# Kernel optimization log

Measured on AMD Instinct MI355X. Metric: run time of the kernel, lower is better.

## Reference

```python
import jax, jax.numpy as jnp
import numpy as np
import math

B, LAT, HID, T, NCLS = 128, 128, 256, 1920, 3
EPS = 1e-5


def _ln(x, g, b):
    m = jnp.mean(x, axis=-1, keepdims=True)
    v = jnp.var(x, axis=-1, keepdims=True)
    return (x - m) * jax.lax.rsqrt(v + EPS) * g + b


def _leaky(x):
    return jax.nn.leaky_relu(x, 0.2)


def _lstm_layer(x, Wih, Whh, bih, bhh):
    # x: [T, B, D] time-major; gate order i,f,g,o (PyTorch convention)
    xw = jnp.einsum('tbd,gd->tbg', x, Wih) + bih + bhh  # precompute input projection
    Hd = Whh.shape[1]
    bsz = x.shape[1]

    def step(carry, xg):
        h, c = carry
        gates = xg + h @ Whh.T
        i, f, g, o = jnp.split(gates, 4, axis=-1)
        c = jax.nn.sigmoid(f) * c + jax.nn.sigmoid(i) * jnp.tanh(g)
        h = jax.nn.sigmoid(o) * jnp.tanh(c)
        return (h, c), h

    init = (jnp.zeros((bsz, Hd), x.dtype), jnp.zeros((bsz, Hd), x.dtype))
    _, hs = jax.lax.scan(step, init, xw)
    return hs  # [T, B, H]


def setup_inputs() -> dict:
    key = jax.random.key(0)
    ks = jax.random.split(key, 16)
    s = 0.05
    H2 = HID // 2
    d = {
        'z': jax.random.normal(ks[0], (B, LAT), jnp.float32),
        'labels': jax.random.randint(ks[1], (B,), 0, 4, jnp.int64),
        'emb_W': jax.random.normal(ks[2], (NCLS + 1, HID), jnp.float32) * s,
        'np_W': jax.random.normal(ks[3], (HID, LAT + HID), jnp.float32) * s,
        'np_b': jnp.zeros((HID,), jnp.float32),
        'np_g': jnp.ones((HID,), jnp.float32),
        'np_be': jnp.zeros((HID,), jnp.float32),
        'Wih0': jax.random.normal(ks[4], (4 * HID, 2 * HID), jnp.float32) * s,
        'Whh0': jax.random.normal(ks[5], (4 * HID, HID), jnp.float32) * s,
        'bih0': jnp.zeros((4 * HID,), jnp.float32),
        'bhh0': jnp.zeros((4 * HID,), jnp.float32),
        'Wih1': jax.random.normal(ks[6], (4 * HID, HID), jnp.float32) * s,
        'Whh1': jax.random.normal(ks[7], (4 * HID, HID), jnp.float32) * s,
        'bih1': jnp.zeros((4 * HID,), jnp.float32),
        'bhh1': jnp.zeros((4 * HID,), jnp.float32),
        'oW1': jax.random.normal(ks[8], (H2, HID), jnp.float32) * s,
        'ob1': jnp.zeros((H2,), jnp.float32),
        'og': jnp.ones((H2,), jnp.float32),
        'obe': jnp.zeros((H2,), jnp.float32),
        'oW2': jax.random.normal(ks[9], (3, H2), jnp.float32) * s,
        'ob2': jnp.zeros((3,), jnp.float32),
        'sW1': jax.random.normal(ks[10], (H2, HID), jnp.float32) * s,
        'sb1': jnp.zeros((H2,), jnp.float32),
        'sg': jnp.ones((H2,), jnp.float32),
        'sbe': jnp.zeros((H2,), jnp.float32),
        'sW2': jax.random.normal(ks[11], (1, H2), jnp.float32) * s,
        'sb2': jnp.zeros((1,), jnp.float32),
        'stress_w': jnp.array(1.8, jnp.float32),
        'amu_w': jnp.array([0.15, 0.7, 0.15], jnp.float32),
        'amu_b': jnp.array(-0.3, jnp.float32),
    }
    return d


def reference(z, labels, emb_W, np_W, np_b, np_g, np_be, Wih0, Whh0, bih0, bhh0,
              Wih1, Whh1, bih1, bhh1, oW1, ob1, og, obe, oW2, ob2,
              sW1, sb1, sg, sbe, sW2, sb2, stress_w, amu_w, amu_b):
    bsz = z.shape[0]
    emb = emb_W[labels]                                   # [B, H]
    h = _leaky(_ln(jnp.concatenate([z, emb], axis=1) @ np_W.T + np_b, np_g, np_be))
    # [B, T, 2H]
    sig_in = jnp.concatenate([
        jnp.broadcast_to(h[:, None, :], (bsz, T, HID)),
        jnp.broadcast_to(emb[:, None, :], (bsz, T, HID)),
    ], axis=2)
    x = jnp.transpose(sig_in, (1, 0, 2))                  # time-major [T, B, 2H]
    x = _lstm_layer(x, Wih0, Whh0, bih0, bhh0)
    x = _lstm_layer(x, Wih1, Whh1, bih1, bhh1)
    ch = jnp.transpose(x, (1, 0, 2))                      # [B, T, H]

    # oscillation params per sample (vectorized over batch)
    h_avg = jnp.mean(ch, axis=1)                          # [B, H]
    op = _leaky(_ln(h_avg @ oW1.T + ob1, og, obe)) @ oW2.T + ob2  # [B, 3]
    freq = 0.23 + 0.04 * jnp.tanh(op[:, 0])
    amp = 2.0 + 1.5 * jnp.tanh(op[:, 1])
    phase = math.pi * jax.nn.sigmoid(op[:, 2])
    t = jnp.linspace(0.0, 1.0, T)
    osc = amp[:, None] * jnp.sin(2.0 * math.pi * freq[:, None] * T * t[None, :] + phase[:, None])  # [B, T]

    base = jnp.tanh(_leaky(_ln(ch @ sW1.T + sb1, sg, sbe)) @ sW2.T + sb2)  # [B, T, 1]
    enhanced = 0.6 * base[..., 0] + 0.4 * osc             # [B, T]

    stressed = stress_w * enhanced                        # conv1d k=1, w=1.8
    xp = jnp.pad(enhanced, ((0, 0), (1, 1)))
    smoothed = amu_w[0] * xp[:, :-2] + amu_w[1] * xp[:, 1:-1] + amu_w[2] * xp[:, 2:] + amu_b

    lab = labels[:, None]
    out = jnp.where(lab == 1, enhanced,
          jnp.where(lab == 2, stressed,
          jnp.where(lab == 3, smoothed, jnp.zeros_like(enhanced))))
    return out[..., None]                                  # [B, T, 1]
```

## Files before the change

kernel.cpp:

```cpp
#include <hip/hip_runtime.h>

#define TSTEPS 1920
#define NB 128
#define HIDN 256
#define LATN 128
#define EPSF 1e-5f

typedef __attribute__((ext_vector_type(8))) short bf16x8;
typedef __attribute__((ext_vector_type(4))) float f32x4;

__device__ __forceinline__ unsigned short f2bf(float x) {
    unsigned u = __builtin_bit_cast(unsigned, x);
    unsigned r = (u + 0x7fffu + ((u >> 16) & 1u)) >> 16;
    return (unsigned short)r;
}
__device__ __forceinline__ float bf2f(unsigned short h) {
    unsigned u = ((unsigned)h) << 16;
    return __builtin_bit_cast(float, u);
}
__device__ __forceinline__ float fsig(float x) {
    float e = __expf(-fabsf(x));
    float s = 1.f / (1.f + e);
    return x >= 0.f ? s : 1.f - s;
}
__device__ __forceinline__ float ftanh(float x) {
    float e = __expf(-2.f * fabsf(x));
    float r = (1.f - e) / (1.f + e);
    return x >= 0.f ? r : -r;
}
__device__ __forceinline__ float fleaky(float x) { return x > 0.f ? x : 0.2f * x; }
__device__ __forceinline__ bf16x8 bcast16(uint4 v) { return __builtin_bit_cast(bf16x8, v); }

__device__ __forceinline__ unsigned aload(const unsigned* p) {
    return __hip_atomic_load(p, __ATOMIC_RELAXED, __HIP_MEMORY_SCOPE_AGENT);
}
__device__ __forceinline__ void astore(unsigned* p, unsigned v) {
    __hip_atomic_store(p, v, __ATOMIC_RELAXED, __HIP_MEMORY_SCOPE_AGENT);
}

#define MFMA(a, b, c) __builtin_amdgcn_mfma_f32_16x16x32_bf16((a), (b), (c), 0, 0, 0)

#define FLG(ph, g, s) (((ph) * 8 + (g)) * 8 + (s)) * 32
#define HPLANE(g, layer, buf) (((g) * 2 + (layer)) * 2 + (buf)) * 4096

__global__ void init_sync(unsigned* hbuf, unsigned* flags) {
    int i = blockIdx.x * 256 + threadIdx.x;
    if (i < 131072) hbuf[i] = 0u;
    if (i < 4096) flags[i] = 0u;
}

__global__ void pack_bfrag_sliced(const float* __restrict__ A, const float* __restrict__ Bsrc,
                                  int KA, int KB,
                                  unsigned short* __restrict__ hi, unsigned short* __restrict__ lo) {
    int e = blockIdx.x * 256 + threadIdx.x;
    int K = KA + KB;
    int KT = K >> 5;
    if (e >= 1024 * K) return;
    int j = e & 7;
    int l = (e >> 3) & 63;
    int r = e >> 9;
    int kt = r % KT;
    int r2 = r / KT;
    int v = r2 & 7;
    int w = r2 >> 3;
    int n = (v >> 1) * 256 + 32 * w + 16 * (v & 1) + (l & 15);
    int k = kt * 32 + (l >> 4) * 8 + j;
    float val = (k < KA) ? A[n * KA + k] : Bsrc[n * KB + (k - KA)];
    unsigned short h = f2bf(val);
    hi[e] = h;
    lo[e] = f2bf(val - bf2f(h));
}

__global__ void pack_sw1kj(const float* __restrict__ sW1, unsigned short* __restrict__ out) {
    int e = blockIdx.x * 256 + threadIdx.x;
    if (e >= 256 * 128) return;
    int j = e & 127, k = e >> 7;
    out[e] = f2bf(sW1[j * 256 + k]);
}

__global__ void pack4T(const float* __restrict__ W, int N, int K, float* __restrict__ out) {
    int e = blockIdx.x * 256 + threadIdx.x;
    if (e >= N * K) return;
    int j = e & 3;
    int rest = e >> 2;
    int n = rest % N;
    int k4 = rest / N;
    out[e] = W[n * K + 4 * k4 + j];
}

__global__ void prep_b1(const float* __restrict__ bih1, const float* __restrict__ bhh1,
                        float* __restrict__ b1sum) {
    int i = blockIdx.x * 256 + threadIdx.x;
    if (i < 1024) b1sum[i] = bih1[i] + bhh1[i];
}

__global__ void np_head(const float* __restrict__ z, const int* __restrict__ labels,
                        const float* __restrict__ emb_W, const float* __restrict__ np_W,
                        const float* __restrict__ np_b, const float* __restrict__ np_g,
                        const float* __restrict__ np_be, float* __restrict__ x_const) {
    int b = blockIdx.x;
    int j = threadIdx.x;
    __shared__ float xc[LATN + HIDN];
    __shared__ float red[8];
    int lab = labels[b];
    if (j < LATN) xc[j] = z[b * LATN + j];
    float e = emb_W[lab * HIDN + j];
    xc[LATN + j] = e;
    __syncthreads();
    float d = np_b[j];
    for (int k = 0; k < LATN + HIDN; ++k) d += xc[k] * np_W[j * (LATN + HIDN) + k];
    int lane = j & 63, wv = j >> 6;
    float s = d, s2 = d * d;
    for (int o = 1; o < 64; o <<= 1) { s += __shfl_xor(s, o); s2 += __shfl_xor(s2, o); }
    if (lane == 0) { red[wv] = s; red[4 + wv] = s2; }
    __syncthreads();
    float S = red[0] + red[1] + red[2] + red[3];
    float S2 = red[4] + red[5] + red[6] + red[7];
    float m = S * (1.f / 256.f);
    float var = S2 * (1.f / 256.f) - m * m;
    float h = fleaky((d - m) * rsqrtf(var + EPSF) * np_g[j] + np_be[j]);
    x_const[b * 512 + j] = h;
    x_const[b * 512 + 256 + j] = e;
}

__global__ void __launch_bounds__(1024) xw0_kernel(const float* __restrict__ x_const,
                                                   const float4* __restrict__ Wih0T4,
                                                   const float* __restrict__ bih0,
                                                   const float* __restrict__ bhh0,
                                                   float* __restrict__ xw0) {
    int b = blockIdx.x;
    int g = threadIdx.x;
    __shared__ float xc[512];
    if (g < 512) xc[g] = x_const[b * 512 + g];
    __syncthreads();
    const float4* xc4 = (const float4*)xc;
    float4 acc = {0.f, 0.f, 0.f, 0.f};
#pragma unroll 8
    for (int k4 = 0; k4 < 128; ++k4) {
        float4 w = Wih0T4[k4 * 1024 + g];
        float4 x = xc4[k4];
        acc.x = fmaf(w.x, x.x, acc.x);
        acc.y = fmaf(w.y, x.y, acc.y);
        acc.z = fmaf(w.z, x.z, acc.z);
        acc.w = fmaf(w.w, x.w, acc.w);
    }
    xw0[b * 1024 + g] = bih0[g] + bhh0[g] + ((acc.x + acc.y) + (acc.z + acc.w));
}

__global__ void __launch_bounds__(512, 2) lstm_coop(
    const uint4* __restrict__ whh0h, const uint4* __restrict__ whh0l,
    const uint4* __restrict__ w1h, const uint4* __restrict__ w1l,
    const unsigned short* __restrict__ sw1kj_g, const float* __restrict__ xw0g,
    const float* __restrict__ b1sum, const float* __restrict__ sb1,
    const float* __restrict__ sg, const float* __restrict__ sbe,
    const float* __restrict__ sW2, const float* __restrict__ sb2,
    unsigned* __restrict__ hbuf, unsigned* __restrict__ flags,
    float* __restrict__ base_out, float* __restrict__ hsum_out) {
    extern __shared__ char smem[];
    unsigned short* hhi = (unsigned short*)smem;
    unsigned short* hlo = (unsigned short*)(smem + 16384);
    unsigned short* sw1s = (unsigned short*)(smem + 32768);
    float* gatesL = (float*)(smem + 98304);
    float* ppart = (float*)(smem + 106752);
    char* hhiB = smem;
    char* hloB = smem + 16384;

    const int gidx = blockIdx.x & 7;
    const int W = blockIdx.x >> 3;
    const int g16 = gidx * 16;
    const int tid = threadIdx.x;
    const int l = tid & 63;
    const int v = tid >> 6;
    const int ln16 = l & 15;
    const int kg = l >> 4;

    for (int i = tid; i < 256 * 128; i += 512) sw1s[i] = sw1kj_g[i];
    for (int i = tid; i < 8192; i += 512) { hhi[i] = 0; hlo[i] = 0; }

    uint4 b0h[8], b0l[8];
#pragma unroll
    for (int kt = 0; kt < 8; ++kt) {
        int idx = ((W * 8 + v) * 8 + kt) * 64 + l;
        b0h[kt] = whh0h[idx];
        b0l[kt] = whh0l[idx];
    }
    const uint4* w1hb = w1h + ((W * 8 + v) * 16) * 64 + l;
    const uint4* w1lb = w1l + ((W * 8 + v) * 16) * 64 + l;

    const int row = tid >> 5;
    const int ul = tid & 31;
    const int ug = 32 * W + ul;
    float xwi[4], b1v[4];
#pragma unroll
    for (int gt = 0; gt < 4; ++gt) {
        xwi[gt] = xw0g[(g16 + row) * 1024 + gt * 256 + ug];
        b1v[gt] = b1sum[gt * 256 + ug];
    }
    float c0 = 0.f, c1 = 0.f, hs = 0.f;

    const float sb1a = sb1[l], sb1b = sb1[64 + l];
    const float sga = sg[l], sgb = sg[64 + l];
    const float sbea = sbe[l], sbeb = sbe[64 + l];
    const float sw2a = sW2[l], sw2b = sW2[64 + l];
    const float sb2v = sb2[0];

    unsigned* h0buf[2] = {hbuf + HPLANE(gidx, 0, 0), hbuf + HPLANE(gidx, 0, 1)};
    unsigned* h1buf[2] = {hbuf + HPLANE(gidx, 1, 0), hbuf + HPLANE(gidx, 1, 1)};
    unsigned* fl0 = flags + FLG(0, gidx, W);
    unsigned* fl1 = flags + FLG(1, gidx, W);
    unsigned* fl0base = flags + FLG(0, gidx, 0);
    unsigned* fl1base = flags + FLG(1, gidx, 0);

    const int abase = ln16 * 1024;
    const int aswz = (ln16 & 7) << 4;
    const int kgo = kg * 16;
    const int gcol = (v >> 1) * 32 + (v & 1) * 16 + ln16;
    const int hprow = 2 * W + (v & 1);
    const int hpswz = (hprow & 7) << 4;
    const int kq = v >> 1;

    __syncthreads();

    for (int t = 0; t < TSTEPS; ++t) {
        const int cur = t & 1, prev = cur ^ 1;
        {
            unsigned* src = h1buf[prev];
            for (int i = tid; i < 4096; i += 512) {
                int r_ = i >> 8, u_ = i & 255;
                unsigned val = aload(src + i);
                int off = r_ * 1024 + ((512 + 2 * u_) ^ ((r_ & 7) << 4));
                *(unsigned short*)(hhiB + off) = (unsigned short)(val >> 16);
                *(unsigned short*)(hloB + off) = (unsigned short)(val & 0xffffu);
            }
        }
        __syncthreads();
        {
            f32x4 acc = {0.f, 0.f, 0.f, 0.f};
#pragma unroll
            for (int kt = 0; kt < 8; ++kt) {
                int aoff = abase + ((kt * 64 + kgo) ^ aswz);
                bf16x8 ahi = bcast16(*(const uint4*)(hhiB + aoff));
                bf16x8 alo = bcast16(*(const uint4*)(hloB + aoff));
                bf16x8 bh = bcast16(b0h[kt]);
                bf16x8 bl = bcast16(b0l[kt]);
                acc = MFMA(ahi, bh, acc);
                acc = MFMA(alo, bh, acc);
                acc = MFMA(ahi, bl, acc);
            }
#pragma unroll
            for (int r = 0; r < 4; ++r) gatesL[(kg * 4 + r) * 132 + gcol] = acc[r];
        }
        if (t > 0) {
            float accA = 0.f, accB = 0.f;
            int hb = hprow * 1024;
#pragma unroll 4
            for (int k = kq * 64; k < kq * 64 + 64; ++k) {
                int off = hb + ((512 + 2 * k) ^ hpswz);
                float h = bf2f(*(const unsigned short*)(hhiB + off)) +
                          bf2f(*(const unsigned short*)(hloB + off));
                float wA = bf2f(sw1s[k * 128 + l]);
                float wB = bf2f(sw1s[k * 128 + 64 + l]);
                accA = fmaf(wA, h, accA);
                accB = fmaf(wB, h, accB);
            }
            ppart[(v & 1) * 512 + kq * 128 + l] = accA;
            ppart[(v & 1) * 512 + kq * 128 + 64 + l] = accB;
        }
        __syncthreads();
        {
            float i_ = gatesL[row * 132 + ul] + xwi[0];
            float f_ = gatesL[row * 132 + 32 + ul] + xwi[1];
            float g_ = gatesL[row * 132 + 64 + ul] + xwi[2];
            float o_ = gatesL[row * 132 + 96 + ul] + xwi[3];
            c0 = fsig(f_) * c0 + fsig(i_) * ftanh(g_);
            float h = fsig(o_) * ftanh(c0);
            unsigned short hh = f2bf(h);
            unsigned short ll = f2bf(h - bf2f(hh));
            astore(h0buf[cur] + row * 256 + ug, ((unsigned)hh << 16) | (unsigned)ll);
        }
        asm volatile("s_waitcnt vmcnt(0)" ::: "memory");
        __syncthreads();
        if (tid == 0) astore(fl0, (unsigned)(t + 1));
        {
            unsigned tgt = (unsigned)(t + 1);
            while (true) {
                unsigned val = (l < 8) ? aload(fl0base + l * 32) : tgt;
                if (__all((int)(val >= tgt))) break;
                __builtin_amdgcn_s_sleep(1);
            }
        }
        asm volatile("" ::: "memory");
        {
            unsigned* src = h0buf[cur];
            for (int i = tid; i < 4096; i += 512) {
                int r_ = i >> 8, u_ = i & 255;
                unsigned val = aload(src + i);
                int off = r_ * 1024 + ((2 * u_) ^ ((r_ & 7) << 4));
                *(unsigned short*)(hhiB + off) = (unsigned short)(val >> 16);
                *(unsigned short*)(hloB + off) = (unsigned short)(val & 0xffffu);
            }
        }
        __syncthreads();
        {
            f32x4 acc = {0.f, 0.f, 0.f, 0.f};
#pragma unroll 4
            for (int kt = 0; kt < 16; ++kt) {
                int aoff = abase + ((kt * 64 + kgo) ^ aswz);
                bf16x8 ahi = bcast16(*(const uint4*)(hhiB + aoff));
                bf16x8 alo = bcast16(*(const uint4*)(hloB + aoff));
                bf16x8 bh = bcast16(w1hb[kt * 64]);
                bf16x8 bl = bcast16(w1lb[kt * 64]);
                acc = MFMA(ahi, bh, acc);
                acc = MFMA(alo, bh, acc);
                acc = MFMA(ahi, bl, acc);
            }
#pragma unroll
            for (int r = 0; r < 4; ++r) gatesL[(kg * 4 + r) * 132 + gcol] = acc[r];
        }
        __syncthreads();
        {
            float i_ = gatesL[row * 132 + ul] + b1v[0];
            float f_ = gatesL[row * 132 + 32 + ul] + b1v[1];
            float g_ = gatesL[row * 132 + 64 + ul] + b1v[2];
            float o_ = gatesL[row * 132 + 96 + ul] + b1v[3];
            c1 = fsig(f_) * c1 + fsig(i_) * ftanh(g_);
            float h = fsig(o_) * ftanh(c1);
            hs += h;
            unsigned short hh = f2bf(h);
            unsigned short ll = f2bf(h - bf2f(hh));
            astore(h1buf[cur] + row * 256 + ug, ((unsigned)hh << 16) | (unsigned)ll);
        }
        if (t > 0 && v < 2) {
            float sA = sb1a, sB = sb1b;
#pragma unroll
            for (int q = 0; q < 4; ++q) {
                sA += ppart[v * 512 + q * 128 + l];
                sB += ppart[v * 512 + q * 128 + 64 + l];
            }
            float ssum = sA + sB, ssq = sA * sA + sB * sB;
#pragma unroll
            for (int o = 1; o < 64; o <<= 1) { ssum += __shfl_xor(ssum, o); ssq += __shfl_xor(ssq, o); }
            float m = ssum * (1.f / 128.f);
            float var = ssq * (1.f / 128.f) - m * m;
            float rstd = rsqrtf(var + EPSF);
            float p0 = fleaky((sA - m) * rstd * sga + sbea);
            float p1 = fleaky((sB - m) * rstd * sgb + sbeb);
            float q = p0 * sw2a + p1 * sw2b;
#pragma unroll
            for (int o = 1; o < 64; o <<= 1) q += __shfl_xor(q, o);
            if (l == 0) base_out[(g16 + 2 * W + v) * TSTEPS + (t - 1)] = ftanh(q + sb2v);
        }
        asm volatile("s_waitcnt vmcnt(0)" ::: "memory");
        __syncthreads();
        if (tid == 0) astore(fl1, (unsigned)(t + 1));
        {
            unsigned tgt = (unsigned)(t + 1);
            while (true) {
                unsigned val = (l < 8) ? aload(fl1base + l * 32) : tgt;
                if (__all((int)(val >= tgt))) break;
                __builtin_amdgcn_s_sleep(1);
            }
        }
        asm volatile("" ::: "memory");
    }
    {
        unsigned* src = h1buf[(TSTEPS - 1) & 1];
        for (int i = tid; i < 4096; i += 512) {
            int r_ = i >> 8, u_ = i & 255;
            unsigned val = aload(src + i);
            int off = r_ * 1024 + ((512 + 2 * u_) ^ ((r_ & 7) << 4));
            *(unsigned short*)(hhiB + off) = (unsigned short)(val >> 16);
            *(unsigned short*)(hloB + off) = (unsigned short)(val & 0xffffu);
        }
    }
    __syncthreads();
    {
        float accA = 0.f, accB = 0.f;
        int hb = hprow * 1024;
#pragma unroll 4
        for (int k = kq * 64; k < kq * 64 + 64; ++k) {
            int off = hb + ((512 + 2 * k) ^ hpswz);
            float h = bf2f(*(const unsigned short*)(hhiB + off)) +
                      bf2f(*(const unsigned short*)(hloB + off));
            accA = fmaf(bf2f(sw1s[k * 128 + l]), h, accA);
            accB = fmaf(bf2f(sw1s[k * 128 + 64 + l]), h, accB);
        }
        ppart[(v & 1) * 512 + kq * 128 + l] = accA;
        ppart[(v & 1) * 512 + kq * 128 + 64 + l] = accB;
    }
    __syncthreads();
    if (v < 2) {
        float sA = sb1a, sB = sb1b;
#pragma unroll
        for (int q = 0; q < 4; ++q) {
            sA += ppart[v * 512 + q * 128 + l];
            sB += ppart[v * 512 + q * 128 + 64 + l];
        }
        float ssum = sA + sB, ssq = sA * sA + sB * sB;
#pragma unroll
        for (int o = 1; o < 64; o <<= 1) { ssum += __shfl_xor(ssum, o); ssq += __shfl_xor(ssq, o); }
        float m = ssum * (1.f / 128.f);
        float var = ssq * (1.f / 128.f) - m * m;
        float rstd = rsqrtf(var + EPSF);
        float p0 = fleaky((sA - m) * rstd * sga + sbea);
        float p1 = fleaky((sB - m) * rstd * sgb + sbeb);
        float q = p0 * sw2a + p1 * sw2b;
#pragma unroll
        for (int o = 1; o < 64; o <<= 1) q += __shfl_xor(q, o);
        if (l == 0) base_out[(g16 + 2 * W + v) * TSTEPS + (TSTEPS - 1)] = ftanh(q + sb2v);
    }
    hsum_out[(g16 + row) * HIDN + ug] = hs;
}

__global__ void out_kernel(const float* __restrict__ hsum, const float* __restrict__ oW1,
                           const float* __restrict__ ob1, const float* __restrict__ og,
                           const float* __restrict__ obe, const float* __restrict__ oW2,
                           const float* __restrict__ ob2, const float* __restrict__ base,
                           const int* __restrict__ labels, const float* __restrict__ stress_w,
                           const float* __restrict__ amu_w, const float* __restrict__ amu_b,
                           float* __restrict__ out) {
    int b = blockIdx.x;
    int tid = threadIdx.x;
    int lane = tid & 63, wv = tid >> 6;
    __shared__ float havg[256];
    __shared__ float red[8];
    __shared__ float params[3];
    __shared__ float e_row[TSTEPS];
    havg[tid] = hsum[b * 256 + tid] * (1.f / (float)TSTEPS);
    __syncthreads();
    float d1 = 0.f;
    if (tid < 128) {
        d1 = ob1[tid];
        for (int k = 0; k < 256; ++k) d1 += havg[k] * oW1[tid * 256 + k];
    }
    float s = d1, s2 = d1 * d1;
    for (int o = 1; o < 64; o <<= 1) { s += __shfl_xor(s, o); s2 += __shfl_xor(s2, o); }
    if (lane == 0 && wv < 2) { red[wv] = s; red[2 + wv] = s2; }
    __syncthreads();
    float m = (red[0] + red[1]) * (1.f / 128.f);
    float var = (red[2] + red[3]) * (1.f / 128.f) - m * m;
    float rstd = rsqrtf(var + EPSF);
    float p = 0.f;
    if (tid < 128) p = fleaky((d1 - m) * rstd * og[tid] + obe[tid]);
    float q0 = tid < 128 ? p * oW2[0 * 128 + tid] : 0.f;
    float q1 = tid < 128 ? p * oW2[1 * 128 + tid] : 0.f;
    float q2 = tid < 128 ? p * oW2[2 * 128 + tid] : 0.f;
    for (int o = 1; o < 64; o <<= 1) {
        q0 += __shfl_xor(q0, o); q1 += __shfl_xor(q1, o); q2 += __shfl_xor(q2, o);
    }
    __syncthreads();
    if (lane == 0 && wv < 2) { red[wv] = q0; red[2 + wv] = q1; red[4 + wv] = q2; }
    __syncthreads();
    if (tid == 0) {
        float op0 = red[0] + red[1] + ob2[0];
        float op1 = red[2] + red[3] + ob2[1];
        float op2 = red[4] + red[5] + ob2[2];
        params[0] = 0.23f + 0.04f * ftanh(op0);
        params[1] = 2.0f + 1.5f * ftanh(op1);
        params[2] = 3.14159265358979f * fsig(op2);
    }
    __syncthreads();
    float freq = params[0], amp = params[1], ph = params[2];
    for (int t = tid; t < TSTEPS; t += 256) {
        float x = freq * ((float)TSTEPS * (float)t / (float)(TSTEPS - 1));
        x -= floorf(x);
        float osc = amp * __sinf(6.28318530717958647f * x + ph);
        e_row[t] = 0.6f * base[b * TSTEPS + t] + 0.4f * osc;
    }
    __syncthreads();
    int lab = labels[b];
    float sw = stress_w[0];
    float w0 = amu_w[0], w1 = amu_w[1], w2 = amu_w[2], ab = amu_b[0];
    for (int t = tid; t < TSTEPS; t += 256) {
        float e = e_row[t];
        float r;
        if (lab == 1) r = e;
        else if (lab == 2) r = sw * e;
        else if (lab == 3) {
            float em = t > 0 ? e_row[t - 1] : 0.f;
            float ep = t < TSTEPS - 1 ? e_row[t + 1] : 0.f;
            r = w0 * em + w1 * e + w2 * ep + ab;
        } else r = 0.f;
        out[b * TSTEPS + t] = r;
    }
}

extern "C" void kernel_launch(void* const* d_in, const int* in_sizes, int n_in,
                              void* d_out, int out_size, void* d_ws, size_t ws_size,
                              hipStream_t stream) {
    (void)in_sizes; (void)n_in; (void)out_size; (void)ws_size;
    const float* z      = (const float*)d_in[0];
    const int* labels   = (const int*)d_in[1];
    const float* emb_W  = (const float*)d_in[2];
    const float* np_W   = (const float*)d_in[3];
    const float* np_b   = (const float*)d_in[4];
    const float* np_g   = (const float*)d_in[5];
    const float* np_be  = (const float*)d_in[6];
    const float* Wih0   = (const float*)d_in[7];
    const float* Whh0   = (const float*)d_in[8];
    const float* bih0   = (const float*)d_in[9];
    const float* bhh0   = (const float*)d_in[10];
    const float* Wih1   = (const float*)d_in[11];
    const float* Whh1   = (const float*)d_in[12];
    const float* bih1   = (const float*)d_in[13];
    const float* bhh1   = (const float*)d_in[14];
    const float* oW1    = (const float*)d_in[15];
    const float* ob1    = (const float*)d_in[16];
    const float* og     = (const float*)d_in[17];
    const float* obe    = (const float*)d_in[18];
    const float* oW2    = (const float*)d_in[19];
    const float* ob2    = (const float*)d_in[20];
    const float* sW1    = (const float*)d_in[21];
    const float* sb1    = (const float*)d_in[22];
    const float* sg     = (const float*)d_in[23];
    const float* sbe    = (const float*)d_in[24];
    const float* sW2    = (const float*)d_in[25];
    const float* sb2    = (const float*)d_in[26];
    const float* stressw= (const float*)d_in[27];
    const float* amu_w  = (const float*)d_in[28];
    const float* amu_b  = (const float*)d_in[29];
    float* out = (float*)d_out;

    uint8_t* ws = (uint8_t*)d_ws;
    size_t off = 0;
    unsigned short* whh0h = (unsigned short*)(ws + off); off += (size_t)1024 * 256 * 2;
    unsigned short* whh0l = (unsigned short*)(ws + off); off += (size_t)1024 * 256 * 2;
    unsigned short* w1h   = (unsigned short*)(ws + off); off += (size_t)1024 * 512 * 2;
    unsigned short* w1l   = (unsigned short*)(ws + off); off += (size_t)1024 * 512 * 2;
    unsigned short* sw1kj = (unsigned short*)(ws + off); off += (size_t)256 * 128 * 2;
    float* Wih0T4 = (float*)(ws + off); off += (size_t)1024 * 512 * 4;
    float* x_const= (float*)(ws + off); off += (size_t)NB * 512 * 4;
    float* xw0    = (float*)(ws + off); off += (size_t)NB * 1024 * 4;
    float* b1sum  = (float*)(ws + off); off += (size_t)1024 * 4;
    float* hsum   = (float*)(ws + off); off += (size_t)NB * 256 * 4;
    float* basef  = (float*)(ws + off); off += (size_t)NB * TSTEPS * 4;
    off = (off + 255) & ~(size_t)255;
    unsigned* hbuf = (unsigned*)(ws + off); off += (size_t)131072 * 4;
    unsigned* flags= (unsigned*)(ws + off); off += (size_t)4096 * 4;

    init_sync<<<512, 256, 0, stream>>>(hbuf, flags);
    pack_bfrag_sliced<<<1024, 256, 0, stream>>>(Whh0, nullptr, 256, 0, whh0h, whh0l);
    pack_bfrag_sliced<<<2048, 256, 0, stream>>>(Wih1, Whh1, 256, 256, w1h, w1l);
    pack_sw1kj<<<128, 256, 0, stream>>>(sW1, sw1kj);
    pack4T<<<2048, 256, 0, stream>>>(Wih0, 1024, 512, Wih0T4);
    prep_b1<<<4, 256, 0, stream>>>(bih1, bhh1, b1sum);

    np_head<<<NB, 256, 0, stream>>>(z, labels, emb_W, np_W, np_b, np_g, np_be, x_const);
    xw0_kernel<<<NB, 1024, 0, stream>>>(x_const, (const float4*)Wih0T4, bih0, bhh0, xw0);
    lstm_coop<<<64, 512, 110848, stream>>>((const uint4*)whh0h, (const uint4*)whh0l,
                                           (const uint4*)w1h, (const uint4*)w1l,
                                           sw1kj, xw0, b1sum, sb1, sg, sbe, sW2, sb2,
                                           hbuf, flags, basef, hsum);
    out_kernel<<<NB, 256, 0, stream>>>(hsum, oW1, ob1, og, obe, oW2, ob2, basef, labels,
                                       stressw, amu_w, amu_b, out);
}
```

Baseline: 23.98 ms.

## Overlap layer-1 Whh partial with layer-0 sync and keep W1 fragments in registers

Restructures the per-timestep schedule of the cooperative LSTM kernel. After a block publishes layer 0, it waits on the layer-1 flag, loads h1(t-1), and computes the Whh1 half of the layer-1 MFMA plus the sigmoid-head dot product before waiting on the layer-0 flag. The separate end-of-step barrier on layer 1 is removed, so each step spends less time spinning on global flags. The W1 bf16 hi/lo fragments are also loaded once into registers instead of from global memory every step, and sW1 is repacked so the head dot product reads 8 values per vector LDS load. The extra register arrays raise VGPR pressure under launch_bounds(512,2) and may cause spills, and the reordered flag protocol has to stay correct across blocks.

```diff
diff --git a/kernel.cpp b/kernel.cpp
--- a/kernel.cpp
+++ b/kernel.cpp
@@ -17,6 +17,12 @@
 __device__ __forceinline__ float bf2f(unsigned short h) {
     unsigned u = ((unsigned)h) << 16;
     return __builtin_bit_cast(float, u);
+}
+__device__ __forceinline__ float u32lo(unsigned w) {
+    return __builtin_bit_cast(float, w << 16);
+}
+__device__ __forceinline__ float u32hi(unsigned w) {
+    return __builtin_bit_cast(float, w & 0xFFFF0000u);
 }
 __device__ __forceinline__ float fsig(float x) {
     float e = __expf(-fabsf(x));
@@ -71,11 +77,11 @@
     lo[e] = f2bf(val - bf2f(h));
 }
 
-__global__ void pack_sw1kj(const float* __restrict__ sW1, unsigned short* __restrict__ out) {
+__global__ void pack_sw1k8(const float* __restrict__ sW1, unsigned short* __restrict__ out) {
     int e = blockIdx.x * 256 + threadIdx.x;
     if (e >= 256 * 128) return;
     int j = e & 127, k = e >> 7;
-    out[e] = f2bf(sW1[j * 256 + k]);
+    out[((k >> 3) * 128 + j) * 8 + (k & 7)] = f2bf(sW1[j * 256 + k]);
 }
 
 __global__ void pack4T(const float* __restrict__ W, int N, int K, float* __restrict__ out) {
@@ -150,7 +156,7 @@
 __global__ void __launch_bounds__(512, 2) lstm_coop(
     const uint4* __restrict__ whh0h, const uint4* __restrict__ whh0l,
     const uint4* __restrict__ w1h, const uint4* __restrict__ w1l,
-    const unsigned short* __restrict__ sw1kj_g, const float* __restrict__ xw0g,
+    const unsigned short* __restrict__ sw1k8_g, const float* __restrict__ xw0g,
     const float* __restrict__ b1sum, const float* __restrict__ sb1,
     const float* __restrict__ sg, const float* __restrict__ sbe,
     const float* __restrict__ sW2, const float* __restrict__ sb2,
@@ -174,7 +180,7 @@
     const int ln16 = l & 15;
     const int kg = l >> 4;
 
-    for (int i = tid; i < 256 * 128; i += 512) sw1s[i] = sw1kj_g[i];
+    for (int i = tid; i < 256 * 128; i += 512) sw1s[i] = sw1k8_g[i];
     for (int i = tid; i < 8192; i += 512) { hhi[i] = 0; hlo[i] = 0; }
 
     uint4 b0h[8], b0l[8];
@@ -184,8 +190,13 @@
         b0h[kt] = whh0h[idx];
         b0l[kt] = whh0l[idx];
     }
-    const uint4* w1hb = w1h + ((W * 8 + v) * 16) * 64 + l;
-    const uint4* w1lb = w1l + ((W * 8 + v) * 16) * 64 + l;
+    uint4 w1hR[16], w1lR[16];
+#pragma unroll
+    for (int kt = 0; kt < 16; ++kt) {
+        int idx = ((W * 8 + v) * 16 + kt) * 64 + l;
+        w1hR[kt] = w1h[idx];
+        w1lR[kt] = w1l[idx];
+    }
 
     const int row = tid >> 5;
     const int ul = tid & 31;
@@ -223,17 +234,6 @@
 
     for (int t = 0; t < TSTEPS; ++t) {
         const int cur = t & 1, prev = cur ^ 1;
-        {
-            unsigned* src = h1buf[prev];
-            for (int i = tid; i < 4096; i += 512) {
-                int r_ = i >> 8, u_ = i & 255;
-                unsigned val = aload(src + i);
-                int off = r_ * 1024 + ((512 + 2 * u_) ^ ((r_ & 7) << 4));
-                *(unsigned short*)(hhiB + off) = (unsigned short)(val >> 16);
-                *(unsigned short*)(hloB + off) = (unsigned short)(val & 0xffffu);
-            }
-        }
-        __syncthreads();
         {
             f32x4 acc = {0.f, 0.f, 0.f, 0.f};
 #pragma unroll
@@ -250,22 +250,6 @@
 #pragma unroll
             for (int r = 0; r < 4; ++r) gatesL[(kg * 4 + r) * 132 + gcol] = acc[r];
         }
-        if (t > 0) {
-            float accA = 0.f, accB = 0.f;
-            int hb = hprow * 1024;
-#pragma unroll 4
-            for (int k = kq * 64; k < kq * 64 + 64; ++k) {
-                int off = hb + ((512 + 2 * k) ^ hpswz);
-                float h = bf2f(*(const unsigned short*)(hhiB + off)) +
-                          bf2f(*(const unsigned short*)(hloB + off));
-                float wA = bf2f(sw1s[k * 128 + l]);
-                float wB = bf2f(sw1s[k * 128 + 64 + l]);
-                accA = fmaf(wA, h, accA);
-                accB = fmaf(wB, h, accB);
-            }
-            ppart[(v & 1) * 512 + kq * 128 + l] = accA;
-            ppart[(v & 1) * 512 + kq * 128 + 64 + l] = accB;
-        }
         __syncthreads();
         {
             float i_ = gatesL[row * 132 + ul] + xwi[0];
@@ -282,6 +266,66 @@
         __syncthreads();
         if (tid == 0) astore(fl0, (unsigned)(t + 1));
         {
+            unsigned tgt = (unsigned)t;
+            while (true) {
+                unsigned val = (l < 8) ? aload(fl1base + l * 32) : tgt;
+                if (__all((int)(val >= tgt))) break;
+                __builtin_amdgcn_s_sleep(1);
+            }
+        }
+        asm volatile("" ::: "memory");
+        {
+            unsigned* src = h1buf[prev];
+            for (int i = tid; i < 4096; i += 512) {
+                int r_ = i >> 8, u_ = i & 255;
+                unsigned val = aload(src + i);
+                int off = r_ * 1024 + ((512 + 2 * u_) ^ ((r_ & 7) << 4));
+                *(unsigned short*)(hhiB + off) = (unsigned short)(val >> 16);
+                *(unsigned short*)(hloB + off) = (unsigned short)(val & 0xffffu);
+            }
+        }
+        __syncthreads();
+        f32x4 acc1 = {0.f, 0.f, 0.f, 0.f};
+#pragma unroll
+        for (int kt = 8; kt < 16; ++kt) {
+            int aoff = abase + ((kt * 64 + kgo) ^ aswz);
+            bf16x8 ahi = bcast16(*(const uint4*)(hhiB + aoff));
+            bf16x8 alo = bcast16(*(const uint4*)(hloB + aoff));
+            bf16x8 bh = bcast16(w1hR[kt]);
+            bf16x8 bl = bcast16(w1lR[kt]);
+            acc1 = MFMA(ahi, bh, acc1);
+            acc1 = MFMA(alo, bh, acc1);
+            acc1 = MFMA(ahi, bl, acc1);
+        }
+        {
+            float accA = 0.f, accB = 0.f;
+            int hb = hprow * 1024;
+#pragma unroll
+            for (int kc = 0; kc < 8; ++kc) {
+                int kb = kq * 64 + kc * 8;
+                uint4 hi4 = *(const uint4*)(hhiB + hb + ((512 + 2 * kb) ^ hpswz));
+                uint4 lo4 = *(const uint4*)(hloB + hb + ((512 + 2 * kb) ^ hpswz));
+                int idx8 = kq * 8 + kc;
+                uint4 wA4 = *(const uint4*)&sw1s[(idx8 * 128 + l) * 8];
+                uint4 wB4 = *(const uint4*)&sw1s[(idx8 * 128 + 64 + l) * 8];
+#pragma unroll
+                for (int q = 0; q < 4; ++q) {
+                    unsigned hw = ((const unsigned*)&hi4)[q];
+                    unsigned lw = ((const unsigned*)&lo4)[q];
+                    float he = u32lo(hw) + u32lo(lw);
+                    float ho = u32hi(hw) + u32hi(lw);
+                    unsigned wa = ((const unsigned*)&wA4)[q];
+                    unsigned wb = ((const unsigned*)&wB4)[q];
+                    accA = fmaf(u32lo(wa), he, accA);
+                    accA = fmaf(u32hi(wa), ho, accA);
+                    accB = fmaf(u32lo(wb), he, accB);
+                    accB = fmaf(u32hi(wb), ho, accB);
+                }
+            }
+            ppart[(v & 1) * 512 + kq * 128 + l] = accA;
+            ppart[(v & 1) * 512 + kq * 128 + 64 + l] = accB;
+        }
+        {
             unsigned tgt = (unsigned)(t + 1);
             while (true) {
                 unsigned val = (l < 8) ? aload(fl0base + l * 32) : tgt;
@@ -302,20 +346,19 @@
         }
         __syncthreads();
         {
-            f32x4 acc = {0.f, 0.f, 0.f, 0.f};
-#pragma unroll 4
-            for (int kt = 0; kt < 16; ++kt) {
+#pragma unroll
+            for (int kt = 0; kt < 8; ++kt) {
                 int aoff = abase + ((kt * 64 + kgo) ^ aswz);
                 bf16x8 ahi = bcast16(*(const uint4*)(hhiB + aoff));
                 bf16x8 alo = bcast16(*(const uint4*)(hloB + aoff));
-                bf16x8 bh = bcast16(w1hb[kt * 64]);
-                bf16x8 bl = bcast16(w1lb[kt * 64]);
-                acc = MFMA(ahi, bh, acc);
-                acc = MFMA(alo, bh, acc);
-                acc = MFMA(ahi, bl, acc);
-            }
-#pragma unroll
-            for (int r = 0; r < 4; ++r) gatesL[(kg * 4 + r) * 132 + gcol] = acc[r];
+                bf16x8 bh = bcast16(w1hR[kt]);
+                bf16x8 bl = bcast16(w1lR[kt]);
+                acc1 = MFMA(ahi, bh, acc1);
+                acc1 = MFMA(alo, bh, acc1);
+                acc1 = MFMA(ahi, bl, acc1);
+            }
+#pragma unroll
+            for (int r = 0; r < 4; ++r) gatesL[(kg * 4 + r) * 132 + gcol] = acc1[r];
         }
         __syncthreads();
         {
@@ -330,6 +373,9 @@
             unsigned short ll = f2bf(h - bf2f(hh));
             astore(h1buf[cur] + row * 256 + ug, ((unsigned)hh << 16) | (unsigned)ll);
         }
+        asm volatile("s_waitcnt vmcnt(0)" ::: "memory");
+        __syncthreads();
+        if (tid == 0) astore(fl1, (unsigned)(t + 1));
         if (t > 0 && v < 2) {
             float sA = sb1a, sB = sb1b;
 #pragma unroll
@@ -350,19 +396,16 @@
             for (int o = 1; o < 64; o <<= 1) q += __shfl_xor(q, o);
             if (l == 0) base_out[(g16 + 2 * W + v) * TSTEPS + (t - 1)] = ftanh(q + sb2v);
         }
-        asm volatile("s_waitcnt vmcnt(0)" ::: "memory");
-        __syncthreads();
-        if (tid == 0) astore(fl1, (unsigned)(t + 1));
-        {
-            unsigned tgt = (unsigned)(t + 1);
-            while (true) {
-                unsigned val = (l < 8) ? aload(fl1base + l * 32) : tgt;
-                if (__all((int)(val >= tgt))) break;
-                __builtin_amdgcn_s_sleep(1);
-            }
-        }
-        asm volatile("" ::: "memory");
-    }
+    }
+    {
+        unsigned tgt = (unsigned)TSTEPS;
+        while (true) {
+            unsigned val = (l < 8) ? aload(fl1base + l * 32) : tgt;
+            if (__all((int)(val >= tgt))) break;
+            __builtin_amdgcn_s_sleep(1);
+        }
+    }
+    asm volatile("" ::: "memory");
     {
         unsigned* src = h1buf[(TSTEPS - 1) & 1];
         for (int i = tid; i < 4096; i += 512) {
@@ -377,13 +420,27 @@
     {
         float accA = 0.f, accB = 0.f;
         int hb = hprow * 1024;
-#pragma unroll 4
-        for (int k = kq * 64; k < kq * 64 + 64; ++k) {
-            int off = hb + ((512 + 2 * k) ^ hpswz);
-            float h = bf2f(*(const unsigned short*)(hhiB + off)) +
-                      bf2f(*(const unsigned short*)(hloB + off));
-            accA = fmaf(bf2f(sw1s[k * 128 + l]), h, accA);
-            accB = fmaf(bf2f(sw1s[k * 128 + 64 + l]), h, accB);
+#pragma unroll
+        for (int kc = 0; kc < 8; ++kc) {
+            int kb = kq * 64 + kc * 8;
+            uint4 hi4 = *(const uint4*)(hhiB + hb + ((512 + 2 * kb) ^ hpswz));
+            uint4 lo4 = *(const uint4*)(hloB + hb + ((512 + 2 * kb) ^ hpswz));
+            int idx8 = kq * 8 + kc;
+            uint4 wA4 = *(const uint4*)&sw1s[(idx8 * 128 + l) * 8];
+            uint4 wB4 = *(const uint4*)&sw1s[(idx8 * 128 + 64 + l) * 8];
+#pragma unroll
+            for (int q = 0; q < 4; ++q) {
+                unsigned hw = ((const unsigned*)&hi4)[q];
+                unsigned lw = ((const unsigned*)&lo4)[q];
+                float he = u32lo(hw) + u32lo(lw);
+                float ho = u32hi(hw) + u32hi(lw);
+                unsigned wa = ((const unsigned*)&wA4)[q];
+                unsigned wb = ((const unsigned*)&wB4)[q];
+                accA = fmaf(u32lo(wa), he, accA);
+                accA = fmaf(u32hi(wa), ho, accA);
+                accB = fmaf(u32lo(wb), he, accB);
+                accB = fmaf(u32hi(wb), ho, accB);
+            }
         }
         ppart[(v & 1) * 512 + kq * 128 + l] = accA;
         ppart[(v & 1) * 512 + kq * 128 + 64 + l] = accB;
@@ -527,7 +584,7 @@
     unsigned short* whh0l = (unsigned short*)(ws + off); off += (size_t)1024 * 256 * 2;
     unsigned short* w1h   = (unsigned short*)(ws + off); off += (size_t)1024 * 512 * 2;
     unsigned short* w1l   = (unsigned short*)(ws + off); off += (size_t)1024 * 512 * 2;
-    unsigned short* sw1kj = (unsigned short*)(ws + off); off += (size_t)256 * 128 * 2;
+    unsigned short* sw1k8 = (unsigned short*)(ws + off); off += (size_t)256 * 128 * 2;
     float* Wih0T4 = (float*)(ws + off); off += (size_t)1024 * 512 * 4;
     float* x_const= (float*)(ws + off); off += (size_t)NB * 512 * 4;
     float* xw0    = (float*)(ws + off); off += (size_t)NB * 1024 * 4;
@@ -541,7 +598,7 @@
     init_sync<<<512, 256, 0, stream>>>(hbuf, flags);
     pack_bfrag_sliced<<<1024, 256, 0, stream>>>(Whh0, nullptr, 256, 0, whh0h, whh0l);
     pack_bfrag_sliced<<<2048, 256, 0, stream>>>(Wih1, Whh1, 256, 256, w1h, w1l);
-    pack_sw1kj<<<128, 256, 0, stream>>>(sW1, sw1kj);
+    pack_sw1k8<<<128, 256, 0, stream>>>(sW1, sw1k8);
     pack4T<<<2048, 256, 0, stream>>>(Wih0, 1024, 512, Wih0T4);
     prep_b1<<<4, 256, 0, stream>>>(bih1, bhh1, b1sum);
 
@@ -549,7 +606,7 @@
     xw0_kernel<<<NB, 1024, 0, stream>>>(x_const, (const float4*)Wih0T4, bih0, bhh0, xw0);
     lstm_coop<<<64, 512, 110848, stream>>>((const uint4*)whh0h, (const uint4*)whh0l,
                                            (const uint4*)w1h, (const uint4*)w1l,
-                                           sw1kj, xw0, b1sum, sb1, sg, sbe, sW2, sb2,
+                                           sw1k8, xw0, b1sum, sb1, sg, sbe, sW2, sb2,
                                            hbuf, flags, basef, hsum);
     out_kernel<<<NB, 256, 0, stream>>>(hsum, oW1, ob1, og, obe, oW2, ob2, basef, labels,
                                        stressw, amu_w, amu_b, out);
```

After: 26.63 ms. 11.1% more time.
